# Optimization experiments

Hardware: AMD Instinct MI355X
Metric: run time of the kernel (lower is better)

Reference implementation:

```python
import jax, jax.numpy as jnp
import numpy as np

INPUT_DIM = 1024
HIDDEN_DIM = 1024
BATCH = 8
SEQ = 2048


def setup_inputs() -> dict:
    key = jax.random.key(0)
    ks = jax.random.split(key, 7)
    s = 1.0 / np.sqrt(INPUT_DIM)
    return {
        "subgraph_embeddings": jax.random.normal(ks[0], (BATCH, SEQ, INPUT_DIM), dtype=jnp.float32),
        "Wq": jax.random.uniform(ks[1], (INPUT_DIM, HIDDEN_DIM), jnp.float32, -s, s),
        "bq": jax.random.uniform(ks[2], (HIDDEN_DIM,), jnp.float32, -s, s),
        "Wk": jax.random.uniform(ks[3], (INPUT_DIM, HIDDEN_DIM), jnp.float32, -s, s),
        "bk": jax.random.uniform(ks[4], (HIDDEN_DIM,), jnp.float32, -s, s),
        "Wv": jax.random.uniform(ks[5], (INPUT_DIM, HIDDEN_DIM), jnp.float32, -s, s),
        "bv": jax.random.uniform(ks[6], (HIDDEN_DIM,), jnp.float32, -s, s),
    }


def reference(subgraph_embeddings, Wq, bq, Wk, bk, Wv, bv):
    x = subgraph_embeddings  # [B, S, D]
    Q = jnp.einsum('bsd,dh->bsh', x, Wq) + bq
    K = jnp.einsum('bsd,dh->bsh', x, Wk) + bk
    V = jnp.einsum('bsd,dh->bsh', x, Wv) + bv
    scale = jnp.sqrt(jnp.float32(HIDDEN_DIM))
    scores = jnp.einsum('bqh,bkh->bqk', Q, K) / scale  # [B, S, S]
    weights = jax.nn.softmax(scores, axis=-1)
    return jnp.einsum('bqk,bkh->bqh', weights, V)
```

## Files before the change

kernel.cpp:

```cpp
#include <hip/hip_runtime.h>
#include <hip/hip_bf16.h>
#include <stdint.h>

typedef unsigned short u16;
typedef unsigned int u32;
typedef __attribute__((ext_vector_type(8))) short bf16x8;
typedef __attribute__((ext_vector_type(4))) float f32x4;

#define S_LEN 2048
#define D_DIM 1024
#define H_DIM 1024
#define BATCH 8
#define M_TOTAL (BATCH * S_LEN)

__device__ __forceinline__ u16 f2b(float f) {
  u32 u = __builtin_bit_cast(u32, f);
  u32 r = (u + 0x7fffu + ((u >> 16) & 1u)) >> 16;
  return (u16)r;
}

__global__ __launch_bounds__(256) void cast_x_kernel(const float* __restrict__ in,
                                                     u16* __restrict__ out, int n8) {
  int i = blockIdx.x * 256 + threadIdx.x;
  if (i >= n8) return;
  const float4* p = (const float4*)in;
  float4 a = p[2 * i], b = p[2 * i + 1];
  u32 w0 = (u32)f2b(a.x) | ((u32)f2b(a.y) << 16);
  u32 w1 = (u32)f2b(a.z) | ((u32)f2b(a.w) << 16);
  u32 w2 = (u32)f2b(b.x) | ((u32)f2b(b.y) << 16);
  u32 w3 = (u32)f2b(b.z) | ((u32)f2b(b.w) << 16);
  ((uint4*)out)[i] = make_uint4(w0, w1, w2, w3);
}

__global__ __launch_bounds__(256) void wcast_all_kernel(
    const float* __restrict__ Wq, const float* __restrict__ Wk,
    const float* __restrict__ Wv, const float* __restrict__ bq,
    const float* __restrict__ bk, u16* __restrict__ Wtqk,
    u16* __restrict__ Wtv, float* __restrict__ bqk, float* __restrict__ lsum) {
  __shared__ float tile[32][33];
  int z = blockIdx.z;
  const float* W = (z == 0) ? Wq : (z == 1) ? Wk : Wv;
  u16* Wt = (z == 0) ? Wtqk : (z == 1) ? (Wtqk + 1024 * 1024) : Wtv;
  int h0 = blockIdx.x * 32, d0 = blockIdx.y * 32;
  int tx = threadIdx.x & 31, ty = threadIdx.x >> 5;
#pragma unroll
  for (int r = ty; r < 32; r += 8)
    tile[r][tx] = W[(size_t)(d0 + r) * H_DIM + h0 + tx];
  if (blockIdx.x == 0 && blockIdx.y == 0) {
    if (z == 0) {
      for (int i = threadIdx.x; i < 1024; i += 256) bqk[i] = bq[i];
    } else if (z == 1) {
      for (int i = threadIdx.x; i < 1024; i += 256) bqk[1024 + i] = bk[i];
    } else {
      for (int i = threadIdx.x; i < M_TOTAL; i += 256) lsum[i] = 0.f;
    }
  }
  __syncthreads();
#pragma unroll
  for (int r = ty; r < 32; r += 8)
    Wt[(size_t)(h0 + r) * D_DIM + d0 + tx] = f2b(tile[tx][r]);
}

template <int BIAS, int EPI, bool OUT_BF16>
__global__ __launch_bounds__(256) void gemm16(
    const u16* __restrict__ A, const u16* __restrict__ Bt, void* __restrict__ Cout,
    const float* __restrict__ bias, float* __restrict__ lsum,
    int M, int N, int K, int lda, int ldb, int ldc,
    long long aBatch, long long bBatch, long long cBatch, float scale) {
  __shared__ __align__(16) u16 As[128 * 64];
  __shared__ __align__(16) u16 Bs[128 * 64];
  const int tid = threadIdx.x;
  const int wave = tid >> 6, lane = tid & 63;
  const int quad = lane >> 4, lr = lane & 15;
  const int wr = (wave >> 1) * 64, wc = (wave & 1) * 64;
  const int row0 = blockIdx.x * 128, col0 = blockIdx.y * 128;
  A += (size_t)blockIdx.z * (size_t)aBatch;
  Bt += (size_t)blockIdx.z * (size_t)bBatch;

  f32x4 acc[4][4] = {};

  auto AsL = (__attribute__((address_space(3))) char*)As;
  auto BsL = (__attribute__((address_space(3))) char*)Bs;
  const char* Ab = (const char*)A;
  const char* Bb = (const char*)Bt;

  for (int k0 = 0; k0 < K; k0 += 64) {
#pragma unroll
    for (int rr = 0; rr < 4; ++rr) {
      int chunk = rr * 256 + tid;
      int row = chunk >> 3;
      int cs = (chunk & 7) ^ (row & 7);
      const void* ga = Ab + (((size_t)(row0 + row) * lda + (size_t)k0 + cs * 8) * 2);
      __builtin_amdgcn_global_load_lds(
          (const __attribute__((address_space(1))) void*)ga,
          (__attribute__((address_space(3))) void*)(AsL + chunk * 16), 16, 0, 0);
      const void* gb = Bb + (((size_t)(col0 + row) * ldb + (size_t)k0 + cs * 8) * 2);
      __builtin_amdgcn_global_load_lds(
          (const __attribute__((address_space(1))) void*)gb,
          (__attribute__((address_space(3))) void*)(BsL + chunk * 16), 16, 0, 0);
    }
    __syncthreads();
#pragma unroll
    for (int ks = 0; ks < 2; ++ks) {
      bf16x8 af[4], bf[4];
#pragma unroll
      for (int i = 0; i < 4; ++i) {
        int r = wr + i * 16 + lr;
        int cc = (ks * 4 + quad) ^ (r & 7);
        af[i] = *(const bf16x8*)&As[r * 64 + cc * 8];
      }
#pragma unroll
      for (int j = 0; j < 4; ++j) {
        int r = wc + j * 16 + lr;
        int cc = (ks * 4 + quad) ^ (r & 7);
        bf[j] = *(const bf16x8*)&Bs[r * 64 + cc * 8];
      }
#pragma unroll
      for (int i = 0; i < 4; ++i)
#pragma unroll
        for (int j = 0; j < 4; ++j)
          acc[i][j] = __builtin_amdgcn_mfma_f32_16x16x32_bf16(af[i], bf[j],
                                                              acc[i][j], 0, 0, 0);
    }
    __syncthreads();
  }

  const long long lrow0 = (long long)blockIdx.z * M + row0;

  if constexpr (EPI == 1) {
    u16* C = (u16*)Cout + (size_t)blockIdx.z * (size_t)cBatch;
#pragma unroll
    for (int i = 0; i < 4; ++i) {
#pragma unroll
      for (int ii = 0; ii < 4; ++ii) {
        int r = wr + i * 16 + quad * 4 + ii;
        float rowsum = 0.f;
#pragma unroll
        for (int j = 0; j < 4; ++j) {
          float e = __expf(acc[i][j][ii] * scale);
          rowsum += e;
          C[(size_t)(row0 + r) * ldc + (col0 + wc + j * 16 + lr)] = f2b(e);
        }
#pragma unroll
        for (int off = 1; off < 16; off <<= 1) rowsum += __shfl_xor(rowsum, off);
        if (lr == 0) atomicAdd(lsum + lrow0 + r, rowsum);
      }
    }
    return;
  }

#pragma unroll
  for (int i = 0; i < 4; ++i) {
#pragma unroll
    for (int ii = 0; ii < 4; ++ii) {
      int r = wr + i * 16 + quad * 4 + ii;
      float radd = 0.f, rmul = 1.f;
      if (BIAS == 2) radd = bias[row0 + r];
      if (EPI == 2) rmul = 1.0f / lsum[lrow0 + r];
#pragma unroll
      for (int j = 0; j < 4; ++j) {
        int c = col0 + wc + j * 16 + lr;
        float v = acc[i][j][ii] * rmul + radd;
        if (BIAS == 1) v += bias[c];
        if constexpr (OUT_BF16) {
          u16* C = (u16*)Cout + (size_t)blockIdx.z * (size_t)cBatch;
          C[(size_t)(row0 + r) * ldc + c] = f2b(v);
        } else {
          float* C = (float*)Cout + (size_t)blockIdx.z * (size_t)cBatch;
          C[(size_t)(row0 + r) * ldc + c] = v;
        }
      }
    }
  }
}

extern "C" void kernel_launch(void* const* d_in, const int* in_sizes, int n_in,
                              void* d_out, int out_size, void* d_ws, size_t ws_size,
                              hipStream_t stream) {
  const float* x = (const float*)d_in[0];
  const float* Wq = (const float*)d_in[1];
  const float* bq = (const float*)d_in[2];
  const float* Wk = (const float*)d_in[3];
  const float* bk = (const float*)d_in[4];
  const float* Wv = (const float*)d_in[5];
  const float* bv = (const float*)d_in[6];
  float* out = (float*)d_out;

  char* ws = (char*)d_ws;
  u16* xb = (u16*)ws;   ws += (size_t)M_TOTAL * D_DIM * 2;
  u16* Wtqk = (u16*)ws; ws += (size_t)2 * H_DIM * D_DIM * 2;
  u16* Wtv = (u16*)ws;  ws += (size_t)H_DIM * D_DIM * 2;
  u16* QKm = (u16*)ws;  ws += (size_t)M_TOTAL * 2 * H_DIM * 2;
  u16* Vt = (u16*)ws;   ws += (size_t)BATCH * H_DIM * S_LEN * 2;
  u16* Sm = (u16*)ws;   ws += (size_t)BATCH * S_LEN * S_LEN * 2;
  float* bqk = (float*)ws;  ws += 2048 * 4;
  float* lsum = (float*)ws; ws += (size_t)M_TOTAL * 4;

  cast_x_kernel<<<(M_TOTAL * D_DIM / 8 + 255) / 256, 256, 0, stream>>>(
      x, xb, M_TOTAL * D_DIM / 8);
  wcast_all_kernel<<<dim3(32, 32, 3), 256, 0, stream>>>(
      Wq, Wk, Wv, bq, bk, Wtqk, Wtv, bqk, lsum);

  gemm16<1, 0, true><<<dim3(128, 16, 1), 256, 0, stream>>>(
      xb, Wtqk, QKm, bqk, nullptr, M_TOTAL, 2 * H_DIM, D_DIM,
      D_DIM, D_DIM, 2 * H_DIM, 0, 0, 0, 0.f);

  gemm16<2, 0, true><<<dim3(8, 16, BATCH), 256, 0, stream>>>(
      Wtv, xb, Vt, bv, nullptr, H_DIM, S_LEN, D_DIM,
      D_DIM, D_DIM, S_LEN,
      0LL, (long long)S_LEN * D_DIM, (long long)H_DIM * S_LEN, 0.f);

  gemm16<0, 1, true><<<dim3(16, 16, BATCH), 256, 0, stream>>>(
      QKm, QKm + H_DIM, Sm, nullptr, lsum, S_LEN, S_LEN, H_DIM,
      2 * H_DIM, 2 * H_DIM, S_LEN,
      (long long)S_LEN * 2 * H_DIM, (long long)S_LEN * 2 * H_DIM,
      (long long)S_LEN * S_LEN, 0.03125f);

  gemm16<0, 2, false><<<dim3(16, 8, BATCH), 256, 0, stream>>>(
      Sm, Vt, out, nullptr, lsum, S_LEN, H_DIM, S_LEN,
      S_LEN, S_LEN, H_DIM,
      (long long)S_LEN * S_LEN, (long long)H_DIM * S_LEN,
      (long long)S_LEN * H_DIM, 0.f);
}
```

Before: 428.2 us.

## Fold Wq·Wkᵀ into a precomputed Gram matrix and drop per-row softmax-invariant bias terms

Replaces the separate Q and K projections with G = Wq·Wkᵀ (a 1024³ GEMM) followed by T = x·G. Scores then become T·xᵀ plus a per-key bias term x·(Wk·bq). Query-only bias terms are dropped because softmax is invariant to per-row constants, and the key-bias vector comes from a small GEMV kernel. This cuts the 2048-wide QK projection to a 1024-wide one plus a small GEMM. In exchange it adds an extra bf16 rounding of G and of T, and it skips the max-subtraction safety as before.

```diff
diff --git a/kernel.cpp b/kernel.cpp
--- a/kernel.cpp
+++ b/kernel.cpp
@@ -18,47 +18,98 @@
   u32 r = (u + 0x7fffu + ((u >> 16) & 1u)) >> 16;
   return (u16)r;
 }
-
-__global__ __launch_bounds__(256) void cast_x_kernel(const float* __restrict__ in,
-                                                     u16* __restrict__ out, int n8) {
-  int i = blockIdx.x * 256 + threadIdx.x;
-  if (i >= n8) return;
-  const float4* p = (const float4*)in;
-  float4 a = p[2 * i], b = p[2 * i + 1];
-  u32 w0 = (u32)f2b(a.x) | ((u32)f2b(a.y) << 16);
-  u32 w1 = (u32)f2b(a.z) | ((u32)f2b(a.w) << 16);
-  u32 w2 = (u32)f2b(b.x) | ((u32)f2b(b.y) << 16);
-  u32 w3 = (u32)f2b(b.z) | ((u32)f2b(b.w) << 16);
-  ((uint4*)out)[i] = make_uint4(w0, w1, w2, w3);
-}
-
-__global__ __launch_bounds__(256) void wcast_all_kernel(
-    const float* __restrict__ Wq, const float* __restrict__ Wk,
-    const float* __restrict__ Wv, const float* __restrict__ bq,
-    const float* __restrict__ bk, u16* __restrict__ Wtqk,
-    u16* __restrict__ Wtv, float* __restrict__ bqk, float* __restrict__ lsum) {
-  __shared__ float tile[32][33];
-  int z = blockIdx.z;
-  const float* W = (z == 0) ? Wq : (z == 1) ? Wk : Wv;
-  u16* Wt = (z == 0) ? Wtqk : (z == 1) ? (Wtqk + 1024 * 1024) : Wtv;
-  int h0 = blockIdx.x * 32, d0 = blockIdx.y * 32;
-  int tx = threadIdx.x & 31, ty = threadIdx.x >> 5;
-#pragma unroll
-  for (int r = ty; r < 32; r += 8)
-    tile[r][tx] = W[(size_t)(d0 + r) * H_DIM + h0 + tx];
-  if (blockIdx.x == 0 && blockIdx.y == 0) {
-    if (z == 0) {
-      for (int i = threadIdx.x; i < 1024; i += 256) bqk[i] = bq[i];
-    } else if (z == 1) {
-      for (int i = threadIdx.x; i < 1024; i += 256) bqk[1024 + i] = bk[i];
+__device__ __forceinline__ float b2f_lo(u32 w) {
+  u32 u = w << 16;
+  return __builtin_bit_cast(float, u);
+}
+__device__ __forceinline__ float b2f_hi(u32 w) {
+  u32 u = w & 0xffff0000u;
+  return __builtin_bit_cast(float, u);
+}
+
+__global__ __launch_bounds__(256) void prep_kernel(
+    const float* __restrict__ x, const float* __restrict__ Wq,
+    const float* __restrict__ Wk, const float* __restrict__ Wv,
+    const float* __restrict__ bq,
+    u16* __restrict__ xb, u16* __restrict__ Wqb, u16* __restrict__ Wkb,
+    u16* __restrict__ Wtv, float* __restrict__ bvec, float* __restrict__ lsum) {
+  int blk = blockIdx.x;
+  if (blk < 9216) {
+    const float* src;
+    u16* dst;
+    int i;
+    if (blk < 8192) {
+      src = x; dst = xb; i = blk * 256 + threadIdx.x;
+    } else if (blk < 8704) {
+      src = Wq; dst = Wqb; i = (blk - 8192) * 256 + threadIdx.x;
+      if (blk == 8192) {
+        for (int t = threadIdx.x; t < M_TOTAL; t += 256) lsum[t] = 0.f;
+      }
     } else {
-      for (int i = threadIdx.x; i < M_TOTAL; i += 256) lsum[i] = 0.f;
-    }
-  }
-  __syncthreads();
-#pragma unroll
-  for (int r = ty; r < 32; r += 8)
-    Wt[(size_t)(h0 + r) * D_DIM + d0 + tx] = f2b(tile[tx][r]);
+      src = Wk; dst = Wkb; i = (blk - 8704) * 256 + threadIdx.x;
+    }
+    const float4* p = (const float4*)src;
+    float4 a = p[2 * i], b = p[2 * i + 1];
+    u32 w0 = (u32)f2b(a.x) | ((u32)f2b(a.y) << 16);
+    u32 w1 = (u32)f2b(a.z) | ((u32)f2b(a.w) << 16);
+    u32 w2 = (u32)f2b(b.x) | ((u32)f2b(b.y) << 16);
+    u32 w3 = (u32)f2b(b.z) | ((u32)f2b(b.w) << 16);
+    ((uint4*)dst)[i] = make_uint4(w0, w1, w2, w3);
+    return;
+  }
+  if (blk < 10240) {
+    __shared__ float tile[32][33];
+    int t = blk - 9216;
+    int h0 = (t & 31) * 32, d0 = (t >> 5) * 32;
+    int tx = threadIdx.x & 31, ty = threadIdx.x >> 5;
+#pragma unroll
+    for (int r = ty; r < 32; r += 8)
+      tile[r][tx] = Wv[(size_t)(d0 + r) * H_DIM + h0 + tx];
+    __syncthreads();
+#pragma unroll
+    for (int r = ty; r < 32; r += 8)
+      Wtv[(size_t)(h0 + r) * D_DIM + d0 + tx] = f2b(tile[tx][r]);
+    return;
+  }
+  int wave = threadIdx.x >> 6, lane = threadIdx.x & 63;
+  int row = (blk - 10240) * 4 + wave;
+  const float4* wr = (const float4*)(Wk + (size_t)row * H_DIM);
+  const float4* br = (const float4*)bq;
+  float s = 0.f;
+#pragma unroll
+  for (int u = 0; u < 4; ++u) {
+    float4 a = wr[lane * 4 + u];
+    float4 b = br[lane * 4 + u];
+    s += a.x * b.x + a.y * b.y + a.z * b.z + a.w * b.w;
+  }
+#pragma unroll
+  for (int off = 1; off < 64; off <<= 1) s += __shfl_xor(s, off);
+  if (lane == 0) bvec[row] = s;
+}
+
+__global__ __launch_bounds__(256) void vvec_kernel(const u16* __restrict__ xb,
+                                                   const float* __restrict__ bvec,
+                                                   float* __restrict__ vb) {
+  int wave = threadIdx.x >> 6, lane = threadIdx.x & 63;
+  int row = blockIdx.x * 4 + wave;
+  const uint4* xr = (const uint4*)(xb + (size_t)row * D_DIM);
+  const float4* br = (const float4*)bvec;
+  float s = 0.f;
+#pragma unroll
+  for (int u = 0; u < 2; ++u) {
+    uint4 q = xr[lane * 2 + u];
+    u32 w[4] = {q.x, q.y, q.z, q.w};
+#pragma unroll
+    for (int k = 0; k < 4; ++k) {
+      float4 b = br[lane * 4 + u * 2 + (k >> 1)];
+      float b0 = (k & 1) ? b.z : b.x;
+      float b1 = (k & 1) ? b.w : b.y;
+      s += b2f_lo(w[k]) * b0 + b2f_hi(w[k]) * b1;
+    }
+  }
+#pragma unroll
+  for (int off = 1; off < 64; off <<= 1) s += __shfl_xor(s, off);
+  if (lane == 0) vb[row] = s * 0.03125f;
 }
 
 template <int BIAS, int EPI, bool OUT_BF16>
@@ -129,6 +180,10 @@
 
   if constexpr (EPI == 1) {
     u16* C = (u16*)Cout + (size_t)blockIdx.z * (size_t)cBatch;
+    float bb[4];
+#pragma unroll
+    for (int j = 0; j < 4; ++j)
+      bb[j] = bias[(long long)blockIdx.z * N + col0 + wc + j * 16 + lr];
 #pragma unroll
     for (int i = 0; i < 4; ++i) {
 #pragma unroll
@@ -137,7 +192,7 @@
         float rowsum = 0.f;
 #pragma unroll
         for (int j = 0; j < 4; ++j) {
-          float e = __expf(acc[i][j][ii] * scale);
+          float e = __expf(acc[i][j][ii] * scale + bb[j]);
           rowsum += e;
           C[(size_t)(row0 + r) * ldc + (col0 + wc + j * 16 + lr)] = f2b(e);
         }
@@ -181,39 +236,45 @@
   const float* Wq = (const float*)d_in[1];
   const float* bq = (const float*)d_in[2];
   const float* Wk = (const float*)d_in[3];
-  const float* bk = (const float*)d_in[4];
   const float* Wv = (const float*)d_in[5];
   const float* bv = (const float*)d_in[6];
   float* out = (float*)d_out;
 
   char* ws = (char*)d_ws;
   u16* xb = (u16*)ws;   ws += (size_t)M_TOTAL * D_DIM * 2;
-  u16* Wtqk = (u16*)ws; ws += (size_t)2 * H_DIM * D_DIM * 2;
+  u16* Wqb = (u16*)ws;  ws += (size_t)D_DIM * H_DIM * 2;
+  u16* Wkb = (u16*)ws;  ws += (size_t)D_DIM * H_DIM * 2;
   u16* Wtv = (u16*)ws;  ws += (size_t)H_DIM * D_DIM * 2;
-  u16* QKm = (u16*)ws;  ws += (size_t)M_TOTAL * 2 * H_DIM * 2;
+  u16* Gt = (u16*)ws;   ws += (size_t)D_DIM * D_DIM * 2;
+  u16* Tm = (u16*)ws;   ws += (size_t)M_TOTAL * D_DIM * 2;
   u16* Vt = (u16*)ws;   ws += (size_t)BATCH * H_DIM * S_LEN * 2;
   u16* Sm = (u16*)ws;   ws += (size_t)BATCH * S_LEN * S_LEN * 2;
-  float* bqk = (float*)ws;  ws += 2048 * 4;
+  float* bvec = (float*)ws; ws += D_DIM * 4;
+  float* vb = (float*)ws;   ws += (size_t)M_TOTAL * 4;
   float* lsum = (float*)ws; ws += (size_t)M_TOTAL * 4;
 
-  cast_x_kernel<<<(M_TOTAL * D_DIM / 8 + 255) / 256, 256, 0, stream>>>(
-      x, xb, M_TOTAL * D_DIM / 8);
-  wcast_all_kernel<<<dim3(32, 32, 3), 256, 0, stream>>>(
-      Wq, Wk, Wv, bq, bk, Wtqk, Wtv, bqk, lsum);
-
-  gemm16<1, 0, true><<<dim3(128, 16, 1), 256, 0, stream>>>(
-      xb, Wtqk, QKm, bqk, nullptr, M_TOTAL, 2 * H_DIM, D_DIM,
-      D_DIM, D_DIM, 2 * H_DIM, 0, 0, 0, 0.f);
+  prep_kernel<<<10496, 256, 0, stream>>>(x, Wq, Wk, Wv, bq, xb, Wqb, Wkb, Wtv,
+                                         bvec, lsum);
+
+  vvec_kernel<<<M_TOTAL / 4, 256, 0, stream>>>(xb, bvec, vb);
+
+  gemm16<0, 0, true><<<dim3(8, 8, 1), 256, 0, stream>>>(
+      Wkb, Wqb, Gt, nullptr, nullptr, 1024, 1024, 1024,
+      1024, 1024, 1024, 0, 0, 0, 0.f);
+
+  gemm16<0, 0, true><<<dim3(128, 8, 1), 256, 0, stream>>>(
+      xb, Gt, Tm, nullptr, nullptr, M_TOTAL, D_DIM, D_DIM,
+      1024, 1024, 1024, 0, 0, 0, 0.f);
 
   gemm16<2, 0, true><<<dim3(8, 16, BATCH), 256, 0, stream>>>(
       Wtv, xb, Vt, bv, nullptr, H_DIM, S_LEN, D_DIM,
-      D_DIM, D_DIM, S_LEN,
+      1024, 1024, S_LEN,
       0LL, (long long)S_LEN * D_DIM, (long long)H_DIM * S_LEN, 0.f);
 
   gemm16<0, 1, true><<<dim3(16, 16, BATCH), 256, 0, stream>>>(
-      QKm, QKm + H_DIM, Sm, nullptr, lsum, S_LEN, S_LEN, H_DIM,
-      2 * H_DIM, 2 * H_DIM, S_LEN,
-      (long long)S_LEN * 2 * H_DIM, (long long)S_LEN * 2 * H_DIM,
+      Tm, xb, Sm, vb, lsum, S_LEN, S_LEN, D_DIM,
+      1024, 1024, S_LEN,
+      (long long)S_LEN * D_DIM, (long long)S_LEN * D_DIM,
       (long long)S_LEN * S_LEN, 0.03125f);
 
   gemm16<0, 2, false><<<dim3(16, 8, BATCH), 256, 0, stream>>>(
```

Result: no change. 431.7 us (+0.8%).
